# Kernel optimization log

Measured on AMD Instinct MI355X. Metric: run time of the kernel, lower is better.

The kernel has to match this reference:

```python
import jax, jax.numpy as jnp
import numpy as np

EMB = 1024
HEADS = 16
HEAD_DIM = EMB // HEADS


def setup_inputs() -> dict:
    key = jax.random.key(0)
    ks = jax.random.split(key, 9)
    s = 1.0 / np.sqrt(EMB)
    x = jax.random.normal(ks[0], (2, 2048, EMB), dtype=jnp.float32)
    Wq = jax.random.normal(ks[1], (EMB, EMB), dtype=jnp.float32) * s
    bq = jnp.zeros((EMB,), dtype=jnp.float32)
    Wk = jax.random.normal(ks[2], (EMB, EMB), dtype=jnp.float32) * s
    bk = jnp.zeros((EMB,), dtype=jnp.float32)
    Wv = jax.random.normal(ks[3], (EMB, EMB), dtype=jnp.float32) * s
    bv = jnp.zeros((EMB,), dtype=jnp.float32)
    Wo = jax.random.normal(ks[4], (EMB, EMB), dtype=jnp.float32) * s
    bo = jnp.zeros((EMB,), dtype=jnp.float32)
    return {"x": x, "Wq": Wq, "bq": bq, "Wk": Wk, "bk": bk,
            "Wv": Wv, "bv": bv, "Wo": Wo, "bo": bo}


def reference(x, Wq, bq, Wk, bk, Wv, bv, Wo, bo):
    B, S, E = x.shape
    # torch Linear: y = x @ W.T + b
    q = x @ Wq.T + bq
    k = x @ Wk.T + bk
    v = x @ Wv.T + bv
    # [B,S,E] -> [B,H,S,D]
    q = q.reshape(B, S, HEADS, HEAD_DIM).transpose(0, 2, 1, 3)
    k = k.reshape(B, S, HEADS, HEAD_DIM).transpose(0, 2, 1, 3)
    v = v.reshape(B, S, HEADS, HEAD_DIM).transpose(0, 2, 1, 3)
    energy = jnp.einsum('bhqd,bhkd->bhqk', q, k)
    scaling = jnp.float32(E) ** 0.5  # NOTE: sqrt(emb_size), not sqrt(head_dim), as in source
    att = jax.nn.softmax(energy / scaling, axis=-1)
    out = jnp.einsum('bhqk,bhkd->bhqd', att, v)
    out = out.transpose(0, 2, 1, 3).reshape(B, S, E)
    return out @ Wo.T + bo
```

## Files before the change

kernel.cpp:

```cpp
#include <hip/hip_runtime.h>
#include <stdint.h>


typedef _Float16 half8  __attribute__((ext_vector_type(8)));
typedef _Float16 half4v __attribute__((ext_vector_type(4)));
typedef _Float16 half2v __attribute__((ext_vector_type(2)));
typedef float    f32x4  __attribute__((ext_vector_type(4)));
typedef float    f32x16 __attribute__((ext_vector_type(16)));

#define GLD16(g, l) __builtin_amdgcn_global_load_lds(                         \
    (__attribute__((address_space(1))) void*)(g),                            \
    (__attribute__((address_space(3))) void*)(l), 16, 0, 0)

#define MFMA16(a, b, c) __builtin_amdgcn_mfma_f32_16x16x32_f16((a), (b), (c), 0, 0, 0)
#define MFMA32(a, b, c) __builtin_amdgcn_mfma_f32_32x32x16_f16((a), (b), (c), 0, 0, 0)

#if __has_builtin(__builtin_amdgcn_exp2f)
#define EXP2(x) __builtin_amdgcn_exp2f(x)
#else
#define EXP2(x) exp2f(x)
#endif

static __device__ inline uint32_t pk_u32(float a, float b)
{
    auto t = __builtin_amdgcn_cvt_pkrtz(a, b);
    return __builtin_bit_cast(uint32_t, t);
}

__global__ void cvt_all(const float* __restrict__ x,  const float* __restrict__ wq,
                        const float* __restrict__ wk, const float* __restrict__ wv,
                        const float* __restrict__ wo, _Float16* __restrict__ xb,
                        _Float16* __restrict__ wqkv, _Float16* __restrict__ wob)
{
    int i = blockIdx.x * blockDim.x + threadIdx.x;
    const float* src; _Float16* dst; int off;
    if (i < 1048576)      { src = x;  dst = xb;                 off = i; }
    else if (i < 1310720) { src = wq; dst = wqkv;               off = i - 1048576; }
    else if (i < 1572864) { src = wk; dst = wqkv + 1048576;     off = i - 1310720; }
    else if (i < 1835008) { src = wv; dst = wqkv + 2097152;     off = i - 1572864; }
    else                  { src = wo; dst = wob;                off = i - 1835008; }
    float4 f = ((const float4*)src)[off];
    half4v h = { (_Float16)f.x, (_Float16)f.y, (_Float16)f.z, (_Float16)f.w };
    ((half4v*)dst)[off] = h;
}

template<int BN, int MODE>
__global__ __launch_bounds__(256, MODE == 0 ? 3 : 2)
void gemm_f16(const _Float16* __restrict__ A, const _Float16* __restrict__ W,
              const float* __restrict__ b0, const float* __restrict__ b1,
              const float* __restrict__ b2, _Float16* __restrict__ o0,
              _Float16* __restrict__ o1, _Float16* __restrict__ o2,
              float* __restrict__ outf, float qscale)
{
    constexpr int NI = BN / 32;
    __shared__ _Float16 lA[128 * 64];
    __shared__ _Float16 lB[BN * 64];
    const int m0 = blockIdx.y * 128, n0 = blockIdx.x * BN;
    const int tid = threadIdx.x, lane = tid & 63, w = tid >> 6;
    const int wr = (w >> 1) * 64, wc = (w & 1) * (BN / 2);
    const int lrow = lane & 15, lk4 = lane >> 4;
    f32x4 acc[4][NI] = {};

    for (int k0 = 0; k0 < 1024; k0 += 64) {
        __syncthreads();
#pragma unroll
        for (int c = 0; c < 4; ++c) {
            int sidx = c * 256 + tid;
            int row = sidx >> 3, sl = sidx & 7;
            int gc = k0 + ((sl ^ (row & 7)) << 3);
            GLD16(A + (size_t)(m0 + row) * 1024 + gc, lA + (size_t)(c * 256 + w * 64) * 8);
        }
#pragma unroll
        for (int c = 0; c < BN / 32; ++c) {
            int sidx = c * 256 + tid;
            int row = sidx >> 3, sl = sidx & 7;
            int gc = k0 + ((sl ^ (row & 7)) << 3);
            GLD16(W + (size_t)(n0 + row) * 1024 + gc, lB + (size_t)(c * 256 + w * 64) * 8);
        }
        __syncthreads();

#pragma unroll
        for (int kd = 0; kd < 2; ++kd) {
            half8 af[4], bf[NI];
#pragma unroll
            for (int mi = 0; mi < 4; ++mi) {
                int ra = wr + mi * 16 + lrow;
                af[mi] = *(const half8*)(lA + ra * 64 + (((kd * 4 + lk4) ^ (ra & 7)) * 8));
            }
#pragma unroll
            for (int ni = 0; ni < NI; ++ni) {
                int rb = wc + ni * 16 + lrow;
                bf[ni] = *(const half8*)(lB + rb * 64 + (((kd * 4 + lk4) ^ (rb & 7)) * 8));
            }
#pragma unroll
            for (int mi = 0; mi < 4; ++mi)
#pragma unroll
                for (int ni = 0; ni < NI; ++ni)
                    acc[mi][ni] = MFMA16(af[mi], bf[ni], acc[mi][ni]);
        }
    }

    if (MODE == 0) {
        const int which = n0 >> 10;
        const float* bp = which == 0 ? b0 : which == 1 ? b1 : b2;
        _Float16* outh  = which == 0 ? o0 : which == 1 ? o1 : o2;
        const float scale = which == 0 ? qscale : 1.f;
        const int nh = n0 & 1023;
        float bcol[NI];
#pragma unroll
        for (int ni = 0; ni < NI; ++ni) bcol[ni] = bp[nh + wc + ni * 16 + lrow];
#pragma unroll
        for (int mi = 0; mi < 4; ++mi)
#pragma unroll
            for (int ni = 0; ni < NI; ++ni)
#pragma unroll
                for (int r = 0; r < 4; ++r) {
                    int rg = m0 + wr + mi * 16 + lk4 * 4 + r;
                    int cg = nh + wc + ni * 16 + lrow;
                    float v = (acc[mi][ni][r] + bcol[ni]) * scale;
                    int b = rg >> 11, s = rg & 2047, h = cg >> 6, d = cg & 63;
                    outh[(((size_t)b * 16 + h) * 2048 + s) * 64 + d] = (_Float16)v;
                }
    } else {
        float bcol[NI];
#pragma unroll
        for (int ni = 0; ni < NI; ++ni) bcol[ni] = b0[n0 + wc + ni * 16 + lrow];
#pragma unroll
        for (int mi = 0; mi < 4; ++mi)
#pragma unroll
            for (int ni = 0; ni < NI; ++ni)
#pragma unroll
                for (int r = 0; r < 4; ++r) {
                    int rg = m0 + wr + mi * 16 + lk4 * 4 + r;
                    int cg = n0 + wc + ni * 16 + lrow;
                    outf[(size_t)rg * 1024 + cg] = acc[mi][ni][r] + bcol[ni];
                }
    }
}

__global__ __launch_bounds__(256)
void transpose_v(const _Float16* __restrict__ v, _Float16* __restrict__ vt)
{
    __shared__ _Float16 t[64][68];
    const int bh = blockIdx.y, s0 = blockIdx.x * 64;
    const _Float16* vh = v + (size_t)bh * 2048 * 64;
    _Float16* vth = vt + (size_t)bh * 64 * 2048;
    const int tid = threadIdx.x;
#pragma unroll
    for (int j = 0; j < 2; ++j) {
        int ch = j * 256 + tid, r = ch >> 3, c = (ch & 7) * 8;
        half8 d = *(const half8*)(vh + (size_t)(s0 + r) * 64 + c);
#pragma unroll
        for (int i = 0; i < 8; ++i) t[r][c + i] = d[i];
    }
    __syncthreads();
#pragma unroll
    for (int j = 0; j < 2; ++j) {
        int ch = j * 256 + tid, d = ch >> 3, sc = (ch & 7) * 8;
        half8 o;
#pragma unroll
        for (int i = 0; i < 8; ++i) o[i] = t[sc + i][d];
        *(half8*)(vth + (size_t)d * 2048 + s0 + sc) = o;
    }
}

#define KVB 64
#define NT  32
__global__ __launch_bounds__(256, 2)
void attn(const _Float16* __restrict__ q, const _Float16* __restrict__ k,
          const _Float16* __restrict__ vt, _Float16* __restrict__ ao)
{
    __shared__ _Float16 lK[2][KVB * 64];
    __shared__ _Float16 lV[2][64 * KVB];
    const int bid0 = blockIdx.x;
    const int bid = (bid0 & 7) * 64 + (bid0 >> 3);
    const int bh = bid >> 4, q0 = (bid & 15) * 128;
    const int bb = bh >> 4, hh = bh & 15;
    const int tid = threadIdx.x, lane = tid & 63, w = tid >> 6;
    const int l31 = lane & 31, h = lane >> 5;
    const _Float16* qh = q + (size_t)bh * 2048 * 64;
    const _Float16* kh = k + (size_t)bh * 2048 * 64;
    const _Float16* vth = vt + (size_t)bh * 64 * 2048;

    half8 qf[4];
#pragma unroll
    for (int kd = 0; kd < 4; ++kd)
        qf[kd] = *(const half8*)(qh + (size_t)(q0 + w * 32 + l31) * 64
                                    + kd * 16 + h * 8);

    float l_ = 0.f;
    f32x16 o0 = {}, o1 = {};

    auto STAGE = [&](int t, int bs) {
        const int s0 = t * KVB;
#pragma unroll
        for (int c = 0; c < 2; ++c) {
            int sidx = c * 256 + tid;
            int row = sidx >> 3, sl = sidx & 7;
            GLD16(kh + (size_t)(s0 + row) * 64 + ((sl ^ (row & 7)) * 8),
                  lK[bs] + (size_t)(c * 256 + w * 64) * 8);
            GLD16(vth + (size_t)row * 2048 + s0 + ((sl ^ (row & 7)) * 8),
                  lV[bs] + (size_t)(c * 256 + w * 64) * 8);
        }
    };

    STAGE(0, 0);
    STAGE(1, 1);

#pragma unroll 2
    for (int t = 0; t < NT; ++t) {
        const int cur = t & 1;
        if (t < NT - 1) asm volatile("s_waitcnt vmcnt(4)" ::: "memory");
        else            asm volatile("s_waitcnt vmcnt(0)" ::: "memory");
        __builtin_amdgcn_s_barrier();
        __builtin_amdgcn_sched_barrier(0);

        f32x16 e0 = {}, e1 = {};
        __builtin_amdgcn_s_setprio(1);
#pragma unroll
        for (int kd = 0; kd < 4; ++kd) {
            int r0 = l31,      s0l = (kd * 2 + h) ^ (r0 & 7);
            int r1 = 32 + l31, s1l = (kd * 2 + h) ^ (r1 & 7);
            half8 kf0 = *(const half8*)(lK[cur] + r0 * 64 + s0l * 8);
            half8 kf1 = *(const half8*)(lK[cur] + r1 * 64 + s1l * 8);
            e0 = MFMA32(kf0, qf[kd], e0);
            e1 = MFMA32(kf1, qf[kd], e1);
        }
        __builtin_amdgcn_s_setprio(0);

        half8 pa[4];
#pragma unroll
        for (int f = 0; f < 2; ++f) {
            float p[16];
#pragma unroll
            for (int r = 0; r < 16; ++r) {
                p[r] = EXP2(f == 0 ? e0[r] : e1[r]);
                l_ += p[r];
            }
#pragma unroll
            for (int bq = 0; bq < 2; ++bq) {
                uint32_t w0 = pk_u32(p[bq * 8 + 0], p[bq * 8 + 1]);
                uint32_t w1 = pk_u32(p[bq * 8 + 2], p[bq * 8 + 3]);
                uint32_t w2 = pk_u32(p[bq * 8 + 4], p[bq * 8 + 5]);
                uint32_t w3 = pk_u32(p[bq * 8 + 6], p[bq * 8 + 7]);
                asm volatile("v_permlane32_swap_b32 %0, %1" : "+v"(w0), "+v"(w2));
                asm volatile("v_permlane32_swap_b32 %0, %1" : "+v"(w1), "+v"(w3));
                union { uint32_t u[4]; half8 hv; } uu;
                uu.u[0] = w0; uu.u[1] = w1; uu.u[2] = w2; uu.u[3] = w3;
                pa[f * 2 + bq] = uu.hv;
            }
        }

        __builtin_amdgcn_s_setprio(1);
#pragma unroll
        for (int ks = 0; ks < 4; ++ks) {
            int r0 = l31,      s0l = (ks * 2 + h) ^ (r0 & 7);
            int r1 = 32 + l31, s1l = (ks * 2 + h) ^ (r1 & 7);
            half8 vf0 = *(const half8*)(lV[cur] + r0 * 64 + s0l * 8);
            half8 vf1 = *(const half8*)(lV[cur] + r1 * 64 + s1l * 8);
            o0 = MFMA32(pa[ks], vf0, o0);
            o1 = MFMA32(pa[ks], vf1, o1);
        }
        __builtin_amdgcn_s_setprio(0);

        __builtin_amdgcn_s_barrier();
        if (t + 2 < NT) STAGE(t + 2, cur);
    }

    l_ += __shfl_xor(l_, 32);
    const size_t obase = ((size_t)bb * 2048) * 1024 + hh * 64;
#pragma unroll
    for (int r = 0; r < 16; ++r) {
        int qr = (r & 3) + 8 * (r >> 2) + 4 * h;
        float linv = 1.f / __shfl(l_, qr);
        int sg = q0 + w * 32 + qr;
        ao[obase + (size_t)sg * 1024 + l31]      = (_Float16)(o0[r] * linv);
        ao[obase + (size_t)sg * 1024 + 32 + l31] = (_Float16)(o1[r] * linv);
    }
}

extern "C" void kernel_launch(void* const* d_in, const int* in_sizes, int n_in,
                              void* d_out, int out_size, void* d_ws, size_t ws_size,
                              hipStream_t stream)
{
    const float* x  = (const float*)d_in[0];
    const float* Wq = (const float*)d_in[1];
    const float* bq = (const float*)d_in[2];
    const float* Wk = (const float*)d_in[3];
    const float* bk = (const float*)d_in[4];
    const float* Wv = (const float*)d_in[5];
    const float* bv = (const float*)d_in[6];
    const float* Wo = (const float*)d_in[7];
    const float* bo = (const float*)d_in[8];
    float* out = (float*)d_out;

    char* ws = (char*)d_ws;
    _Float16* xb   = (_Float16*)(ws);
    _Float16* vtb  = (_Float16*)(ws);
    _Float16* wqkv = (_Float16*)(ws + (8u  << 20));
    _Float16* wob  = (_Float16*)(ws + (14u << 20));
    _Float16* qb   = (_Float16*)(ws + (16u << 20));
    _Float16* kb   = (_Float16*)(ws + (24u << 20));
    _Float16* vb   = (_Float16*)(ws + (32u << 20));
    _Float16* aob  = vb;

    cvt_all<<<8192, 256, 0, stream>>>(x, Wq, Wk, Wv, Wo, xb, wqkv, wob);

    const float qscale = 1.4426950408889634f / 32.f;
    gemm_f16<128, 0><<<dim3(24, 32), 256, 0, stream>>>(
        xb, wqkv, bq, bk, bv, qb, kb, vb, nullptr, qscale);

    transpose_v<<<dim3(32, 32), 256, 0, stream>>>(vb, vtb);

    attn<<<512, 256, 0, stream>>>(qb, kb, vtb, aob);

    gemm_f16<64, 1><<<dim3(16, 32), 256, 0, stream>>>(
        aob, wob, bo, nullptr, nullptr, nullptr, nullptr, nullptr, out, 1.f);
}
```

Baseline: 114.3 us.

## Fuse V transpose into QKV GEMM epilogue and triple-buffer attention K/V staging

The QKV GEMM epilogue now writes V directly in transposed [b,h,d,s] layout using packed 4-half stores, so the separate transpose_v kernel and its extra launch and memory round trip go away. The attention kernel moves from double to triple LDS buffering. The next tile's prefetch is issued right after the barrier, which drops the second barrier per iteration. All K/V fragments are loaded into registers up front, and the softmax/PV work is split into two halves so the second exp can overlap the first PV MFMAs. This uses more LDS and registers, which may affect the two-blocks-per-CU occupancy target.

Measured after the change: 106.4 us. -7.0%, faster.

```diff
diff --git a/kernel.cpp b/kernel.cpp
--- a/kernel.cpp
+++ b/kernel.cpp
@@ -103,24 +103,41 @@
     if (MODE == 0) {
         const int which = n0 >> 10;
         const float* bp = which == 0 ? b0 : which == 1 ? b1 : b2;
-        _Float16* outh  = which == 0 ? o0 : which == 1 ? o1 : o2;
         const float scale = which == 0 ? qscale : 1.f;
         const int nh = n0 & 1023;
         float bcol[NI];
 #pragma unroll
         for (int ni = 0; ni < NI; ++ni) bcol[ni] = bp[nh + wc + ni * 16 + lrow];
-#pragma unroll
-        for (int mi = 0; mi < 4; ++mi)
-#pragma unroll
-            for (int ni = 0; ni < NI; ++ni)
-#pragma unroll
-                for (int r = 0; r < 4; ++r) {
-                    int rg = m0 + wr + mi * 16 + lk4 * 4 + r;
+        if (which == 2) {
+#pragma unroll
+            for (int mi = 0; mi < 4; ++mi)
+#pragma unroll
+                for (int ni = 0; ni < NI; ++ni) {
                     int cg = nh + wc + ni * 16 + lrow;
-                    float v = (acc[mi][ni][r] + bcol[ni]) * scale;
-                    int b = rg >> 11, s = rg & 2047, h = cg >> 6, d = cg & 63;
-                    outh[(((size_t)b * 16 + h) * 2048 + s) * 64 + d] = (_Float16)v;
+                    int hh = cg >> 6, dd = cg & 63;
+                    int sb = m0 + wr + mi * 16 + lk4 * 4;
+                    int bb = sb >> 11, ss = sb & 2047;
+                    half4v pkv;
+#pragma unroll
+                    for (int r = 0; r < 4; ++r)
+                        pkv[r] = (_Float16)(acc[mi][ni][r] + bcol[ni]);
+                    *(half4v*)(o2 + ((size_t)(bb * 16 + hh) * 64 + dd) * 2048 + ss) = pkv;
                 }
+        } else {
+            _Float16* outh = which == 0 ? o0 : o1;
+#pragma unroll
+            for (int mi = 0; mi < 4; ++mi)
+#pragma unroll
+                for (int ni = 0; ni < NI; ++ni)
+#pragma unroll
+                    for (int r = 0; r < 4; ++r) {
+                        int rg = m0 + wr + mi * 16 + lk4 * 4 + r;
+                        int cg = nh + wc + ni * 16 + lrow;
+                        float v = (acc[mi][ni][r] + bcol[ni]) * scale;
+                        int b = rg >> 11, s = rg & 2047, hh = cg >> 6, dd = cg & 63;
+                        outh[(((size_t)b * 16 + hh) * 2048 + s) * 64 + dd] = (_Float16)v;
+                    }
+        }
     } else {
         float bcol[NI];
 #pragma unroll
@@ -138,40 +155,14 @@
     }
 }
 
-__global__ __launch_bounds__(256)
-void transpose_v(const _Float16* __restrict__ v, _Float16* __restrict__ vt)
-{
-    __shared__ _Float16 t[64][68];
-    const int bh = blockIdx.y, s0 = blockIdx.x * 64;
-    const _Float16* vh = v + (size_t)bh * 2048 * 64;
-    _Float16* vth = vt + (size_t)bh * 64 * 2048;
-    const int tid = threadIdx.x;
-#pragma unroll
-    for (int j = 0; j < 2; ++j) {
-        int ch = j * 256 + tid, r = ch >> 3, c = (ch & 7) * 8;
-        half8 d = *(const half8*)(vh + (size_t)(s0 + r) * 64 + c);
-#pragma unroll
-        for (int i = 0; i < 8; ++i) t[r][c + i] = d[i];
-    }
-    __syncthreads();
-#pragma unroll
-    for (int j = 0; j < 2; ++j) {
-        int ch = j * 256 + tid, d = ch >> 3, sc = (ch & 7) * 8;
-        half8 o;
-#pragma unroll
-        for (int i = 0; i < 8; ++i) o[i] = t[sc + i][d];
-        *(half8*)(vth + (size_t)d * 2048 + s0 + sc) = o;
-    }
-}
-
 #define KVB 64
 #define NT  32
 __global__ __launch_bounds__(256, 2)
 void attn(const _Float16* __restrict__ q, const _Float16* __restrict__ k,
           const _Float16* __restrict__ vt, _Float16* __restrict__ ao)
 {
-    __shared__ _Float16 lK[2][KVB * 64];
-    __shared__ _Float16 lV[2][64 * KVB];
+    __shared__ _Float16 lKf[3 * KVB * 64];
+    __shared__ _Float16 lVf[3 * 64 * KVB];
     const int bid0 = blockIdx.x;
     const int bid = (bid0 & 7) * 64 + (bid0 >> 3);
     const int bh = bid >> 4, q0 = (bid & 15) * 128;
@@ -193,50 +184,65 @@
 
     auto STAGE = [&](int t, int bs) {
         const int s0 = t * KVB;
+        _Float16* Kd = lKf + bs * (KVB * 64);
+        _Float16* Vd = lVf + bs * (64 * KVB);
 #pragma unroll
         for (int c = 0; c < 2; ++c) {
             int sidx = c * 256 + tid;
             int row = sidx >> 3, sl = sidx & 7;
             GLD16(kh + (size_t)(s0 + row) * 64 + ((sl ^ (row & 7)) * 8),
-                  lK[bs] + (size_t)(c * 256 + w * 64) * 8);
+                  Kd + (size_t)(c * 256 + w * 64) * 8);
             GLD16(vth + (size_t)row * 2048 + s0 + ((sl ^ (row & 7)) * 8),
-                  lV[bs] + (size_t)(c * 256 + w * 64) * 8);
+                  Vd + (size_t)(c * 256 + w * 64) * 8);
         }
     };
 
     STAGE(0, 0);
     STAGE(1, 1);
 
-#pragma unroll 2
     for (int t = 0; t < NT; ++t) {
-        const int cur = t & 1;
+        const int cur = t % 3;
         if (t < NT - 1) asm volatile("s_waitcnt vmcnt(4)" ::: "memory");
         else            asm volatile("s_waitcnt vmcnt(0)" ::: "memory");
         __builtin_amdgcn_s_barrier();
         __builtin_amdgcn_sched_barrier(0);
+        if (t + 2 < NT) STAGE(t + 2, (t + 2) % 3);
+
+        const _Float16* Kb = lKf + cur * (KVB * 64);
+        const _Float16* Vb = lVf + cur * (64 * KVB);
+
+        half8 kf[8], vf[8];
+#pragma unroll
+        for (int kd = 0; kd < 4; ++kd) {
+            int s0l = (kd * 2 + h) ^ (l31 & 7);
+            int s1l = (kd * 2 + h) ^ ((32 + l31) & 7);
+            kf[kd * 2]     = *(const half8*)(Kb + l31 * 64 + s0l * 8);
+            kf[kd * 2 + 1] = *(const half8*)(Kb + (32 + l31) * 64 + s1l * 8);
+        }
+#pragma unroll
+        for (int ks = 0; ks < 4; ++ks) {
+            int s0l = (ks * 2 + h) ^ (l31 & 7);
+            int s1l = (ks * 2 + h) ^ ((32 + l31) & 7);
+            vf[ks * 2]     = *(const half8*)(Vb + l31 * 64 + s0l * 8);
+            vf[ks * 2 + 1] = *(const half8*)(Vb + (32 + l31) * 64 + s1l * 8);
+        }
 
         f32x16 e0 = {}, e1 = {};
         __builtin_amdgcn_s_setprio(1);
 #pragma unroll
         for (int kd = 0; kd < 4; ++kd) {
-            int r0 = l31,      s0l = (kd * 2 + h) ^ (r0 & 7);
-            int r1 = 32 + l31, s1l = (kd * 2 + h) ^ (r1 & 7);
-            half8 kf0 = *(const half8*)(lK[cur] + r0 * 64 + s0l * 8);
-            half8 kf1 = *(const half8*)(lK[cur] + r1 * 64 + s1l * 8);
-            e0 = MFMA32(kf0, qf[kd], e0);
-            e1 = MFMA32(kf1, qf[kd], e1);
+            e0 = MFMA32(kf[kd * 2], qf[kd], e0);
+            e1 = MFMA32(kf[kd * 2 + 1], qf[kd], e1);
         }
         __builtin_amdgcn_s_setprio(0);
 
         half8 pa[4];
-#pragma unroll
-        for (int f = 0; f < 2; ++f) {
+        {
             float p[16];
 #pragma unroll
-            for (int r = 0; r < 16; ++r) {
-                p[r] = EXP2(f == 0 ? e0[r] : e1[r]);
-                l_ += p[r];
-            }
+            for (int r = 0; r < 16; ++r) p[r] = EXP2(e0[r]);
+            l_ += (((p[0] + p[1]) + (p[2] + p[3])) + ((p[4] + p[5]) + (p[6] + p[7])))
+                + (((p[8] + p[9]) + (p[10] + p[11])) + ((p[12] + p[13]) + (p[14] + p[15])));
 #pragma unroll
             for (int bq = 0; bq < 2; ++bq) {
                 uint32_t w0 = pk_u32(p[bq * 8 + 0], p[bq * 8 + 1]);
@@ -247,24 +253,45 @@
                 asm volatile("v_permlane32_swap_b32 %0, %1" : "+v"(w1), "+v"(w3));
                 union { uint32_t u[4]; half8 hv; } uu;
                 uu.u[0] = w0; uu.u[1] = w1; uu.u[2] = w2; uu.u[3] = w3;
-                pa[f * 2 + bq] = uu.hv;
+                pa[bq] = uu.hv;
             }
         }
 
         __builtin_amdgcn_s_setprio(1);
 #pragma unroll
-        for (int ks = 0; ks < 4; ++ks) {
-            int r0 = l31,      s0l = (ks * 2 + h) ^ (r0 & 7);
-            int r1 = 32 + l31, s1l = (ks * 2 + h) ^ (r1 & 7);
-            half8 vf0 = *(const half8*)(lV[cur] + r0 * 64 + s0l * 8);
-            half8 vf1 = *(const half8*)(lV[cur] + r1 * 64 + s1l * 8);
-            o0 = MFMA32(pa[ks], vf0, o0);
-            o1 = MFMA32(pa[ks], vf1, o1);
+        for (int ks = 0; ks < 2; ++ks) {
+            o0 = MFMA32(pa[ks], vf[ks * 2], o0);
+            o1 = MFMA32(pa[ks], vf[ks * 2 + 1], o1);
         }
         __builtin_amdgcn_s_setprio(0);
 
-        __builtin_amdgcn_s_barrier();
-        if (t + 2 < NT) STAGE(t + 2, cur);
+        {
+            float p[16];
+#pragma unroll
+            for (int r = 0; r < 16; ++r) p[r] = EXP2(e1[r]);
+            l_ += (((p[0] + p[1]) + (p[2] + p[3])) + ((p[4] + p[5]) + (p[6] + p[7])))
+                + (((p[8] + p[9]) + (p[10] + p[11])) + ((p[12] + p[13]) + (p[14] + p[15])));
+#pragma unroll
+            for (int bq = 0; bq < 2; ++bq) {
+                uint32_t w0 = pk_u32(p[bq * 8 + 0], p[bq * 8 + 1]);
+                uint32_t w1 = pk_u32(p[bq * 8 + 2], p[bq * 8 + 3]);
+                uint32_t w2 = pk_u32(p[bq * 8 + 4], p[bq * 8 + 5]);
+                uint32_t w3 = pk_u32(p[bq * 8 + 6], p[bq * 8 + 7]);
+                asm volatile("v_permlane32_swap_b32 %0, %1" : "+v"(w0), "+v"(w2));
+                asm volatile("v_permlane32_swap_b32 %0, %1" : "+v"(w1), "+v"(w3));
+                union { uint32_t u[4]; half8 hv; } uu;
+                uu.u[0] = w0; uu.u[1] = w1; uu.u[2] = w2; uu.u[3] = w3;
+                pa[2 + bq] = uu.hv;
+            }
+        }
+
+        __builtin_amdgcn_s_setprio(1);
+#pragma unroll
+        for (int ks = 2; ks < 4; ++ks) {
+            o0 = MFMA32(pa[ks], vf[ks * 2], o0);
+            o1 = MFMA32(pa[ks], vf[ks * 2 + 1], o1);
+        }
+        __builtin_amdgcn_s_setprio(0);
     }
 
     l_ += __shfl_xor(l_, 32);
@@ -296,21 +323,18 @@
 
     char* ws = (char*)d_ws;
     _Float16* xb   = (_Float16*)(ws);
-    _Float16* vtb  = (_Float16*)(ws);
+    _Float16* aob  = xb;
     _Float16* wqkv = (_Float16*)(ws + (8u  << 20));
     _Float16* wob  = (_Float16*)(ws + (14u << 20));
     _Float16* qb   = (_Float16*)(ws + (16u << 20));
     _Float16* kb   = (_Float16*)(ws + (24u << 20));
-    _Float16* vb   = (_Float16*)(ws + (32u << 20));
-    _Float16* aob  = vb;
+    _Float16* vtb  = (_Float16*)(ws + (32u << 20));
 
     cvt_all<<<8192, 256, 0, stream>>>(x, Wq, Wk, Wv, Wo, xb, wqkv, wob);
 
     const float qscale = 1.4426950408889634f / 32.f;
     gemm_f16<128, 0><<<dim3(24, 32), 256, 0, stream>>>(
-        xb, wqkv, bq, bk, bv, qb, kb, vb, nullptr, qscale);
-
-    transpose_v<<<dim3(32, 32), 256, 0, stream>>>(vb, vtb);
+        xb, wqkv, bq, bk, bv, qb, kb, vtb, nullptr, qscale);
 
     attn<<<512, 256, 0, stream>>>(qb, kb, vtb, aob);
 
```
